# Performance work log

Measured on AMD Instinct MI355X. Metric: run time of the kernel, lower is better.

Reference implementation:

```python
import jax, jax.numpy as jnp
import numpy as np

GRID_SIZE = 5
SPLINE_ORDER = 3
GRID_RANGE = (-1.0, 1.0)
LAYERS = [1024, 1024, 1024]
BATCH = 8192
LN_EPS = 1e-5


def _make_grid(in_features):
    h = (GRID_RANGE[1] - GRID_RANGE[0]) / GRID_SIZE
    n = GRID_SIZE + 2 * SPLINE_ORDER + 1  # 12 knots
    g = jnp.linspace(GRID_RANGE[0] - h * SPLINE_ORDER,
                     GRID_RANGE[1] + h * SPLINE_ORDER, n, dtype=jnp.float32)
    return jnp.broadcast_to(g, (in_features, n))


def setup_inputs() -> dict:
    key = jax.random.key(0)
    ks = jax.random.split(key, 8)
    n_layers = len(LAYERS) - 1
    d_in, d_out = LAYERS[0], LAYERS[1]  # square layers -> stackable params
    coeff = GRID_SIZE + SPLINE_ORDER  # 8
    # kaiming_uniform_(nonlinearity='linear'): bound = sqrt(3) * (1/sqrt(fan_in))
    bw_bound = float(np.sqrt(3.0) / np.sqrt(d_in))
    sw_bound = float(np.sqrt(3.0) / np.sqrt(d_in * coeff))
    x = jax.random.normal(ks[0], (BATCH, d_in), dtype=jnp.float32)
    base_w = jax.random.uniform(ks[1], (n_layers, d_out, d_in), jnp.float32, -bw_bound, bw_bound)
    spline_w = jax.random.uniform(ks[2], (n_layers, d_out, d_in, coeff), jnp.float32, -sw_bound, sw_bound)
    ln_g = jnp.ones((n_layers, d_out), jnp.float32)
    ln_b = jnp.zeros((n_layers, d_out), jnp.float32)
    prelu_a = jnp.full((n_layers,), 0.25, jnp.float32)
    grid = jnp.stack([_make_grid(d_in) for _ in range(n_layers)])  # [L, in, 12]
    return {"x": x, "base_w": base_w, "spline_w": spline_w,
            "ln_g": ln_g, "ln_b": ln_b, "prelu_a": prelu_a, "grid": grid}


def _bspline_bases(x, g):
    """Cox-de Boor recursion. x: [B, in], g: [in, n_knots] -> [B, in, G+order]."""
    xu = x[..., None]  # [B, in, 1]
    bases = ((xu >= g[:, :-1]) & (xu < g[:, 1:])).astype(x.dtype)  # [B, in, 11]
    for k in range(1, SPLINE_ORDER + 1):
        left = g[:, :-(k + 1)]
        right = g[:, k:-1]
        delta = jnp.where(right == left, jnp.ones_like(right), right - left)
        bases = ((xu - left) / delta * bases[..., :-1]
                 + (g[:, k + 1:] - xu) / (g[:, k + 1:] - g[:, 1:-k]) * bases[..., 1:])
    return bases  # [B, in, 8]


def kan_forward(x, base_w, spline_w, ln_g, ln_b, prelu_a, grid):
    n_layers = base_w.shape[0]
    for i in range(n_layers):
        base_out = jnp.matmul(jax.nn.gelu(x, approximate=False), base_w[i].T)  # [B, out]
        bases = _bspline_bases(x, grid[i])  # [B, in, 8]
        spline_out = jnp.matmul(bases.reshape(x.shape[0], -1),
                                spline_w[i].reshape(spline_w.shape[1], -1).T)  # [B, out]
        h = base_out + spline_out
        mu = jnp.mean(h, axis=-1, keepdims=True)
        var = jnp.var(h, axis=-1, keepdims=True)  # biased, matches torch LayerNorm
        h = (h - mu) * jax.lax.rsqrt(var + LN_EPS) * ln_g[i] + ln_b[i]
        x = jnp.where(h >= 0, h, prelu_a[i] * h)  # PReLU (scalar slope per layer)
    return x


def reference(x, base_w, spline_w, ln_g, ln_b, prelu_a, grid):
    return kan_forward(x, base_w, spline_w, ln_g, ln_b, prelu_a, grid)
```

## Files before the change

kernel.cpp:

```cpp
#include <hip/hip_runtime.h>
#include <hip/hip_bf16.h>
#include <cstdint>
#include <cstddef>

typedef __bf16 bf16_t;
typedef __bf16 bf16x8 __attribute__((ext_vector_type(8)));
typedef __bf16 bf16x4 __attribute__((ext_vector_type(4)));
typedef float  f32x4  __attribute__((ext_vector_type(4)));

#define DIM    1024
#define NCOEF  8
#define KTOT   (DIM + DIM * NCOEF)
#define NKNOT  12
#define BATCH  8192
#define LN_EPS 1e-5f

__device__ __forceinline__ float gelu_exact(float x) {
    return 0.5f * x * (1.0f + erff(x * 0.70710678118654752440f));
}

__device__ __forceinline__ void gl_lds16(const void* g, void* l) {
    __builtin_amdgcn_global_load_lds(
        (const __attribute__((address_space(1))) unsigned int*)(uintptr_t)g,
        (__attribute__((address_space(3))) unsigned int*)(uintptr_t)l, 16, 0, 0);
}

__device__ __forceinline__ uint64_t pack4bf(float a, float b, float c, float d) {
    union { bf16_t h[4]; uint64_t q; } u;
    u.h[0] = (bf16_t)a; u.h[1] = (bf16_t)b; u.h[2] = (bf16_t)c; u.h[3] = (bf16_t)d;
    return u.q;
}

__device__ __forceinline__ void spline8(float x, float g0, float invh,
                                        uint64_t& lo, uint64_t& hi) {
    float u = (x - g0) * invh;
    float jf = floorf(u);
    int j = (int)jf;
    float f = u - jf;
    float f2 = f * f, f3 = f2 * f;
    float om = 1.0f - f, om2 = om * om;
    float w0 = om2 * om * (1.0f / 6.0f);
    float w3 = f3 * (1.0f / 6.0f);
    float w1 = fmaf(0.5f, f3, 2.0f / 3.0f) - f2;
    float w2 = 1.0f - w0 - w1 - w3;
    uint64_t W64 = pack4bf(w0, w1, w2, w3);
    if (!(u >= 0.0f && u < 11.0f)) W64 = 0;
    int sh = (j - 3) * 16;
    if (sh >= 0) {
        int s = sh & 63;
        uint64_t loW = W64 << s;
        uint64_t hiW = s ? (W64 >> (64 - s)) : 0ull;
        lo = (sh < 64) ? loW : 0ull;
        hi = (sh < 64) ? hiW : loW;
    } else {
        lo = W64 >> (-sh);
        hi = 0ull;
    }
}

__global__ void pack_w(const float* __restrict__ bw, const float* __restrict__ sw,
                       bf16_t* __restrict__ W) {
    int idx = blockIdx.x * 256 + threadIdx.x;
    bf16_t* wrow = W + (size_t)(idx >> 10) * KTOT;
    int j = idx & 1023;
    wrow[j] = (bf16_t)bw[idx];
    const float4* sp = (const float4*)(sw + (size_t)idx * NCOEF);
    float4 s0 = sp[0], s1 = sp[1];
    bf16x8 v;
    v[0] = (bf16_t)s0.x; v[1] = (bf16_t)s0.y; v[2] = (bf16_t)s0.z; v[3] = (bf16_t)s0.w;
    v[4] = (bf16_t)s1.x; v[5] = (bf16_t)s1.y; v[6] = (bf16_t)s1.z; v[7] = (bf16_t)s1.w;
    *(bf16x8*)(wrow + DIM + j * NCOEF) = v;
}

__global__ void prep_A(const float* __restrict__ x, bf16_t* __restrict__ A,
                       const float* __restrict__ gp) {
    const int row = blockIdx.x, t = threadIdx.x;
    const float g0 = gp[0];
    const float invh = 1.0f / (gp[1] - gp[0]);
    f32x4 v = *(const f32x4*)(x + (size_t)row * DIM + t * 4);
    bf16_t* Ar = A + (size_t)row * KTOT;
    bf16x4 ge;
#pragma unroll
    for (int k = 0; k < 4; k++) ge[k] = (bf16_t)gelu_exact(v[k]);
    *(bf16x4*)(Ar + t * 4) = ge;
#pragma unroll
    for (int k = 0; k < 4; k++) {
        uint64_t lo, hi;
        union { uint64_t u[2]; uint4 q; } o;
        spline8(v[k], g0, invh, lo, hi);
        o.u[0] = lo; o.u[1] = hi;
        *(uint4*)(Ar + DIM + (t * 4 + k) * NCOEF) = o.q;
    }
}


#define STAGE(T, S) { \
    const size_t ko_ = (size_t)(T) * 32; \
    gl_lds16(Ag0 + ko_, ldsA + (S) * 8192 + tid * 8); \
    gl_lds16(Ag1 + ko_, ldsA + (S) * 8192 + 4096 + tid * 8); \
    gl_lds16(Bg0 + ko_, ldsB + (S) * 8192 + tid * 8); \
    gl_lds16(Bg1 + ko_, ldsB + (S) * 8192 + 4096 + tid * 8); }

#define MF_ROW(I, A_) \
    acc[I][0] = __builtin_amdgcn_mfma_f32_16x16x32_bf16(A_, b0_, acc[I][0], 0, 0, 0); \
    acc[I][1] = __builtin_amdgcn_mfma_f32_16x16x32_bf16(A_, b1_, acc[I][1], 0, 0, 0); \
    acc[I][2] = __builtin_amdgcn_mfma_f32_16x16x32_bf16(A_, b2_, acc[I][2], 0, 0, 0); \
    acc[I][3] = __builtin_amdgcn_mfma_f32_16x16x32_bf16(A_, b3_, acc[I][3], 0, 0, 0);

#define TILE_COMPUTE(S) { \
    const bf16_t* Bb_ = ldsB + (S) * 8192 + bOff; \
    bf16x8 b0_ = *(const bf16x8*)(Bb_),        b1_ = *(const bf16x8*)(Bb_ + 512), \
           b2_ = *(const bf16x8*)(Bb_ + 1024), b3_ = *(const bf16x8*)(Bb_ + 1536); \
    const bf16_t* Ab_ = ldsA + (S) * 8192 + aOff; \
    { bf16x8 a0_ = *(const bf16x8*)(Ab_),        a1_ = *(const bf16x8*)(Ab_ + 512), \
             a2_ = *(const bf16x8*)(Ab_ + 1024), a3_ = *(const bf16x8*)(Ab_ + 1536); \
      __builtin_amdgcn_s_setprio(1); \
      MF_ROW(0, a0_) MF_ROW(1, a1_) MF_ROW(2, a2_) MF_ROW(3, a3_) \
      __builtin_amdgcn_s_setprio(0); } \
    { bf16x8 a4_ = *(const bf16x8*)(Ab_ + 2048), a5_ = *(const bf16x8*)(Ab_ + 2560), \
             a6_ = *(const bf16x8*)(Ab_ + 3072), a7_ = *(const bf16x8*)(Ab_ + 3584); \
      __builtin_amdgcn_s_setprio(1); \
      MF_ROW(4, a4_) MF_ROW(5, a5_) MF_ROW(6, a6_) MF_ROW(7, a7_) \
      __builtin_amdgcn_s_setprio(0); } }

#define BAR() { __builtin_amdgcn_s_barrier(); asm volatile("" ::: "memory"); }

#define TILE_MAIN(T, S, SP) { \
    STAGE((T) + 2, SP) \
    asm volatile("s_waitcnt vmcnt(8)" ::: "memory"); \
    BAR() \
    TILE_COMPUTE(S) }

template<int NTK>
__global__ __launch_bounds__(512, 2) void gemm_ab(
    const bf16_t* __restrict__ A,
    const bf16_t* __restrict__ W,
    float* __restrict__ C,
    int mmask, int mshift, int rows) {
    __shared__ __align__(16) bf16_t lds[65536];
    bf16_t* __restrict__ ldsA = lds;
    bf16_t* __restrict__ ldsB = lds + 32768;

    const int tid = threadIdx.x;
    const int l = tid & 63, wv = tid >> 6;
    const int wm = wv >> 2, wn = wv & 3;

    const int chunk = gridDim.x >> 3;
    const int bid = blockIdx.x;
    const int wg = (bid & 7) * chunk + (bid >> 3);
    const int bm = wg & mmask;
    const int bn = (wg >> mshift) & 3;
    const int ks = wg >> (mshift + 2);
    const int row0 = bm << 8, col0 = bn << 8;
    const int koff0 = ks * (NTK * 32);

    const int srow = tid >> 2;
    const int slc = (tid & 3) ^ ((srow >> 1) & 3);
    const bf16_t* __restrict__ Ag0 = A + (size_t)(row0 + srow) * KTOT + koff0 + slc * 8;
    const bf16_t* __restrict__ Ag1 = Ag0 + (size_t)128 * KTOT;
    const bf16_t* __restrict__ Bg0 = W + (size_t)(col0 + srow) * KTOT + koff0 + slc * 8;
    const bf16_t* __restrict__ Bg1 = Bg0 + (size_t)128 * KTOT;

    const int l15 = l & 15;
    const int pc = (l >> 4) ^ ((l15 >> 1) & 3);
    const int aOff = (wm * 128 + l15) * 32 + pc * 8;
    const int bOff = (wn * 64 + l15) * 32 + pc * 8;

    f32x4 acc[8][4] = {};

    STAGE(0, 0)
    STAGE(1, 1)
#pragma unroll 1
    for (int t = 0; t < NTK - 4; t += 4) {
        TILE_MAIN(t,     0, 2)
        TILE_MAIN(t + 1, 1, 3)
        TILE_MAIN(t + 2, 2, 0)
        TILE_MAIN(t + 3, 3, 1)
    }
    TILE_MAIN(NTK - 4, 0, 2)
    TILE_MAIN(NTK - 3, 1, 3)
    asm volatile("s_waitcnt vmcnt(4)" ::: "memory");
    BAR()
    TILE_COMPUTE(2)
    asm volatile("s_waitcnt vmcnt(0)" ::: "memory");
    BAR()
    TILE_COMPUTE(3)

    float* __restrict__ Cp = C + (size_t)ks * rows * DIM;
    const int r0 = row0 + wm * 128 + (l >> 4) * 4;
    const int c0 = col0 + wn * 64 + l15;
#pragma unroll
    for (int i = 0; i < 8; i++)
#pragma unroll
        for (int j = 0; j < 4; j++)
#pragma unroll
            for (int r = 0; r < 4; r++)
                Cp[(size_t)(r0 + i * 16 + r) * DIM + c0 + j * 16] = acc[i][j][r];
}

__global__ void ln_mid_A(const float* __restrict__ h, int rows, int ksplit,
                         const float* __restrict__ g_ln, const float* __restrict__ b_ln,
                         const float* __restrict__ pa, bf16_t* __restrict__ A,
                         const float* __restrict__ gp) {
    const int row = blockIdx.x, tid = threadIdx.x;
    const int w = tid >> 6, l = tid & 63;
    f32x4 v = {0.0f, 0.0f, 0.0f, 0.0f};
    for (int ks = 0; ks < ksplit; ks++)
        v += *(const f32x4*)(h + ((size_t)ks * rows + row) * DIM + tid * 4);
    float s = v[0] + v[1] + v[2] + v[3];
    float q = v[0] * v[0] + v[1] * v[1] + v[2] * v[2] + v[3] * v[3];
#pragma unroll
    for (int o = 32; o > 0; o >>= 1) { s += __shfl_xor(s, o); q += __shfl_xor(q, o); }
    __shared__ float rs[4], rq[4];
    if (l == 0) { rs[w] = s; rq[w] = q; }
    __syncthreads();
    s = rs[0] + rs[1] + rs[2] + rs[3];
    q = rq[0] + rq[1] + rq[2] + rq[3];
    float mean = s * (1.0f / DIM);
    float var = q * (1.0f / DIM) - mean * mean;
    float rstd = rsqrtf(var + LN_EPS);
    float a = pa[0];
    const float g0 = gp[0];
    const float invh = 1.0f / (gp[1] - gp[0]);
    bf16_t* Ar = A + (size_t)row * KTOT;
    bf16x4 ge;
#pragma unroll
    for (int c = 0; c < 4; c++) {
        int col = tid * 4 + c;
        float yv = (v[c] - mean) * rstd * g_ln[col] + b_ln[col];
        yv = (yv >= 0.0f) ? yv : a * yv;
        ge[c] = (bf16_t)gelu_exact(yv);
        uint64_t lo, hi;
        union { uint64_t u[2]; uint4 qv; } o;
        spline8(yv, g0, invh, lo, hi);
        o.u[0] = lo; o.u[1] = hi;
        *(uint4*)(Ar + DIM + (size_t)col * NCOEF) = o.qv;
    }
    *(bf16x4*)(Ar + tid * 4) = ge;
}

__global__ void ln_out(const float* __restrict__ h, int rows, int ksplit,
                       const float* __restrict__ g_ln, const float* __restrict__ b_ln,
                       const float* __restrict__ pa, float* __restrict__ out) {
    const int row = blockIdx.x, tid = threadIdx.x;
    const int w = tid >> 6, l = tid & 63;
    f32x4 v = {0.0f, 0.0f, 0.0f, 0.0f};
    for (int ks = 0; ks < ksplit; ks++)
        v += *(const f32x4*)(h + ((size_t)ks * rows + row) * DIM + tid * 4);
    float s = v[0] + v[1] + v[2] + v[3];
    float q = v[0] * v[0] + v[1] * v[1] + v[2] * v[2] + v[3] * v[3];
#pragma unroll
    for (int o = 32; o > 0; o >>= 1) { s += __shfl_xor(s, o); q += __shfl_xor(q, o); }
    __shared__ float rs[4], rq[4];
    if (l == 0) { rs[w] = s; rq[w] = q; }
    __syncthreads();
    s = rs[0] + rs[1] + rs[2] + rs[3];
    q = rq[0] + rq[1] + rq[2] + rq[3];
    float mean = s * (1.0f / DIM);
    float var = q * (1.0f / DIM) - mean * mean;
    float rstd = rsqrtf(var + LN_EPS);
    float a = pa[0];
    f32x4 o4;
#pragma unroll
    for (int c = 0; c < 4; c++) {
        int col = tid * 4 + c;
        float yv = (v[c] - mean) * rstd * g_ln[col] + b_ln[col];
        o4[c] = (yv >= 0.0f) ? yv : a * yv;
    }
    *(f32x4*)(out + (size_t)row * DIM + tid * 4) = o4;
}

extern "C" void kernel_launch(void* const* d_in, const int* in_sizes, int n_in,
                              void* d_out, int out_size, void* d_ws, size_t ws_size,
                              hipStream_t stream) {
    const float* x    = (const float*)d_in[0];
    const float* bw   = (const float*)d_in[1];
    const float* sw   = (const float*)d_in[2];
    const float* ln_g = (const float*)d_in[3];
    const float* ln_b = (const float*)d_in[4];
    const float* pa   = (const float*)d_in[5];
    const float* gridK = (const float*)d_in[6];
    float* out = (float*)d_out;

    const size_t wbytes = (size_t)2 * DIM * KTOT * sizeof(bf16_t);
    int R = 8192, ksplit = 2;
    for (;;) {
        size_t need = wbytes + (size_t)R * KTOT * 2 + (size_t)ksplit * R * DIM * 4;
        if (need <= ws_size || R == 512) break;
        R >>= 1;
        int mt = R / 256;
        ksplit = (mt >= 32) ? 2 : (mt >= 16) ? 4 : 8;
    }
    int mtiles = R / 256;
    int mshift = 0; while ((1 << mshift) < mtiles) mshift++;
    int mmask = mtiles - 1;
    int grid = mtiles * 4 * ksplit;

    char* wsc = (char*)d_ws;
    bf16_t* Wbuf = (bf16_t*)wsc;
    bf16_t* Abuf = (bf16_t*)(wsc + wbytes);
    float*  hbuf = (float*)(wsc + wbytes + (size_t)R * KTOT * 2);

    pack_w<<<(2 * DIM * DIM) / 256, 256, 0, stream>>>(bw, sw, Wbuf);

    auto launch_gemm = [&](const bf16_t* Wl, hipStream_t st) {
        if (ksplit == 2)
            gemm_ab<144><<<grid, 512, 0, st>>>(Abuf, Wl, hbuf, mmask, mshift, R);
        else if (ksplit == 4)
            gemm_ab<72><<<grid, 512, 0, st>>>(Abuf, Wl, hbuf, mmask, mshift, R);
        else
            gemm_ab<36><<<grid, 512, 0, st>>>(Abuf, Wl, hbuf, mmask, mshift, R);
    };

    const int nslab = BATCH / R;
    for (int sidx = 0; sidx < nslab; sidx++) {
        const size_t row0 = (size_t)sidx * R;
        const float* x0 = x + row0 * DIM;
        prep_A<<<R, 256, 0, stream>>>(x0, Abuf, gridK);
        launch_gemm(Wbuf, stream);
        ln_mid_A<<<R, 256, 0, stream>>>(hbuf, R, ksplit, ln_g, ln_b, pa,
                                        Abuf, gridK + DIM * NKNOT);
        launch_gemm(Wbuf + (size_t)DIM * KTOT, stream);
        ln_out<<<R, 256, 0, stream>>>(hbuf, R, ksplit, ln_g + DIM, ln_b + DIM,
                                      pa + 1, out + row0 * DIM);
    }
}
```

Baseline: 574.1 us.

## Deepen GEMM LDS pipeline to three stages with split half-tile barriers

```diff
diff --git a/kernel.cpp b/kernel.cpp
--- a/kernel.cpp
+++ b/kernel.cpp
@@ -94,42 +94,56 @@
 }
 
 
-#define STAGE(T, S) { \
-    const size_t ko_ = (size_t)(T) * 32; \
-    gl_lds16(Ag0 + ko_, ldsA + (S) * 8192 + tid * 8); \
-    gl_lds16(Ag1 + ko_, ldsA + (S) * 8192 + 4096 + tid * 8); \
-    gl_lds16(Bg0 + ko_, ldsB + (S) * 8192 + tid * 8); \
-    gl_lds16(Bg1 + ko_, ldsB + (S) * 8192 + 4096 + tid * 8); }
+#define STR2(x) #x
+#define GATEV(N) asm volatile("s_waitcnt vmcnt(" STR2(N) ")" ::: "memory");
 
 #define MF_ROW(I, A_) \
-    acc[I][0] = __builtin_amdgcn_mfma_f32_16x16x32_bf16(A_, b0_, acc[I][0], 0, 0, 0); \
-    acc[I][1] = __builtin_amdgcn_mfma_f32_16x16x32_bf16(A_, b1_, acc[I][1], 0, 0, 0); \
-    acc[I][2] = __builtin_amdgcn_mfma_f32_16x16x32_bf16(A_, b2_, acc[I][2], 0, 0, 0); \
-    acc[I][3] = __builtin_amdgcn_mfma_f32_16x16x32_bf16(A_, b3_, acc[I][3], 0, 0, 0);
-
-#define TILE_COMPUTE(S) { \
-    const bf16_t* Bb_ = ldsB + (S) * 8192 + bOff; \
-    bf16x8 b0_ = *(const bf16x8*)(Bb_),        b1_ = *(const bf16x8*)(Bb_ + 512), \
-           b2_ = *(const bf16x8*)(Bb_ + 1024), b3_ = *(const bf16x8*)(Bb_ + 1536); \
-    const bf16_t* Ab_ = ldsA + (S) * 8192 + aOff; \
-    { bf16x8 a0_ = *(const bf16x8*)(Ab_),        a1_ = *(const bf16x8*)(Ab_ + 512), \
-             a2_ = *(const bf16x8*)(Ab_ + 1024), a3_ = *(const bf16x8*)(Ab_ + 1536); \
-      __builtin_amdgcn_s_setprio(1); \
-      MF_ROW(0, a0_) MF_ROW(1, a1_) MF_ROW(2, a2_) MF_ROW(3, a3_) \
-      __builtin_amdgcn_s_setprio(0); } \
-    { bf16x8 a4_ = *(const bf16x8*)(Ab_ + 2048), a5_ = *(const bf16x8*)(Ab_ + 2560), \
-             a6_ = *(const bf16x8*)(Ab_ + 3072), a7_ = *(const bf16x8*)(Ab_ + 3584); \
-      __builtin_amdgcn_s_setprio(1); \
-      MF_ROW(4, a4_) MF_ROW(5, a5_) MF_ROW(6, a6_) MF_ROW(7, a7_) \
-      __builtin_amdgcn_s_setprio(0); } }
-
-#define BAR() { __builtin_amdgcn_s_barrier(); asm volatile("" ::: "memory"); }
-
-#define TILE_MAIN(T, S, SP) { \
-    STAGE((T) + 2, SP) \
-    asm volatile("s_waitcnt vmcnt(8)" ::: "memory"); \
-    BAR() \
-    TILE_COMPUTE(S) }
+    acc[I][0] = __builtin_amdgcn_mfma_f32_16x16x32_bf16(A_, b0, acc[I][0], 0, 0, 0); \
+    acc[I][1] = __builtin_amdgcn_mfma_f32_16x16x32_bf16(A_, b1, acc[I][1], 0, 0, 0); \
+    acc[I][2] = __builtin_amdgcn_mfma_f32_16x16x32_bf16(A_, b2, acc[I][2], 0, 0, 0); \
+    acc[I][3] = __builtin_amdgcn_mfma_f32_16x16x32_bf16(A_, b3, acc[I][3], 0, 0, 0);
+
+#define TILE(T, S, SP, DOSTAGE, GATESTMT) { \
+    bf16x8 a0, a1, a2, a3, a4, a5, a6, a7, b0, b1, b2, b3; \
+     \
+    { const bf16_t* Ab_ = ldsA + (S) * 8192 + aOff; \
+      const bf16_t* Bb_ = ldsB + (S) * 8192 + bOff; \
+      a0 = *(const bf16x8*)(Ab_);        a1 = *(const bf16x8*)(Ab_ + 512); \
+      a2 = *(const bf16x8*)(Ab_ + 1024); a3 = *(const bf16x8*)(Ab_ + 1536); \
+      b0 = *(const bf16x8*)(Bb_);        b1 = *(const bf16x8*)(Bb_ + 512); \
+      b2 = *(const bf16x8*)(Bb_ + 1024); b3 = *(const bf16x8*)(Bb_ + 1536); } \
+    if (DOSTAGE) { \
+      gl_lds16(Ag0 + (size_t)((T) + 3) * 32, ldsA + (SP) * 8192 + tid * 8); \
+      gl_lds16(Ag1 + (size_t)((T) + 3) * 32, ldsA + (SP) * 8192 + 4096 + tid * 8); } \
+    __builtin_amdgcn_s_barrier(); \
+    asm volatile("s_waitcnt lgkmcnt(0)" ::: "memory"); \
+    __builtin_amdgcn_sched_barrier(0); \
+    __builtin_amdgcn_s_setprio(1); \
+    MF_ROW(0, a0) MF_ROW(1, a1) MF_ROW(2, a2) MF_ROW(3, a3) \
+    __builtin_amdgcn_s_setprio(0); \
+    __builtin_amdgcn_s_barrier(); \
+     \
+    { const bf16_t* Ab_ = ldsA + (S) * 8192 + aOff; \
+      a4 = *(const bf16x8*)(Ab_ + 2048); a5 = *(const bf16x8*)(Ab_ + 2560); \
+      a6 = *(const bf16x8*)(Ab_ + 3072); a7 = *(const bf16x8*)(Ab_ + 3584); } \
+    if (DOSTAGE) { \
+      gl_lds16(Bg0 + (size_t)((T) + 3) * 32, ldsB + (SP) * 8192 + tid * 8); \
+      gl_lds16(Bg1 + (size_t)((T) + 3) * 32, ldsB + (SP) * 8192 + 4096 + tid * 8); } \
+    GATESTMT \
+    __builtin_amdgcn_s_barrier(); \
+    asm volatile("s_waitcnt lgkmcnt(0)" ::: "memory"); \
+    __builtin_amdgcn_sched_barrier(0); \
+    __builtin_amdgcn_s_setprio(1); \
+    MF_ROW(4, a4) MF_ROW(5, a5) MF_ROW(6, a6) MF_ROW(7, a7) \
+    __builtin_amdgcn_s_setprio(0); \
+    __builtin_amdgcn_s_barrier(); \
+}
+
+#define PSTAGE(T, S) \
+    gl_lds16(Ag0 + (size_t)(T) * 32, ldsA + (S) * 8192 + tid * 8); \
+    gl_lds16(Ag1 + (size_t)(T) * 32, ldsA + (S) * 8192 + 4096 + tid * 8); \
+    gl_lds16(Bg0 + (size_t)(T) * 32, ldsB + (S) * 8192 + tid * 8); \
+    gl_lds16(Bg1 + (size_t)(T) * 32, ldsB + (S) * 8192 + 4096 + tid * 8);
 
 template<int NTK>
 __global__ __launch_bounds__(512, 2) void gemm_ab(
@@ -168,23 +182,23 @@
 
     f32x4 acc[8][4] = {};
 
-    STAGE(0, 0)
-    STAGE(1, 1)
+    PSTAGE(0, 0)
+    PSTAGE(1, 1)
+    PSTAGE(2, 2)
+    GATEV(8)
+    __builtin_amdgcn_s_barrier();
+
 #pragma unroll 1
     for (int t = 0; t < NTK - 4; t += 4) {
-        TILE_MAIN(t,     0, 2)
-        TILE_MAIN(t + 1, 1, 3)
-        TILE_MAIN(t + 2, 2, 0)
-        TILE_MAIN(t + 3, 3, 1)
-    }
-    TILE_MAIN(NTK - 4, 0, 2)
-    TILE_MAIN(NTK - 3, 1, 3)
-    asm volatile("s_waitcnt vmcnt(4)" ::: "memory");
-    BAR()
-    TILE_COMPUTE(2)
-    asm volatile("s_waitcnt vmcnt(0)" ::: "memory");
-    BAR()
-    TILE_COMPUTE(3)
+        TILE(t + 0, 0, 3, 1, GATEV(8))
+        TILE(t + 1, 1, 0, 1, GATEV(8))
+        TILE(t + 2, 2, 1, 1, GATEV(8))
+        TILE(t + 3, 3, 2, 1, GATEV(8))
+    }
+    TILE(NTK - 4, 0, 3, 1, GATEV(8))
+    TILE(NTK - 3, 1, 0, 0, GATEV(4))
+    TILE(NTK - 2, 2, 0, 0, GATEV(0))
+    TILE(NTK - 1, 3, 0, 0, ;)
 
     float* __restrict__ Cp = C + (size_t)ks * rows * DIM;
     const int r0 = row0 + wm * 128 + (l >> 4) * 4;
```

After: 566.2 us. Within noise of the previous version (-1.4%).
